# Kernel optimization log

Hardware: AMD Instinct MI355X
Metric: run time of the kernel (lower is better)

## Reference

```python
import jax, jax.numpy as jnp
import numpy as np

EPS = 1e-08
N_NODES = 100000
E_HALF = 3200000  # directed edges before symmetrization


def setup_inputs() -> dict:
    key = jax.random.key(0)
    k1, k2, k3 = jax.random.split(key, 3)
    pos = jax.random.normal(k1, (N_NODES, 3), dtype=jnp.float32)
    phi = jax.random.normal(k2, (N_NODES,), dtype=jnp.float32)
    e = jax.random.randint(k3, (2, E_HALF), 0, N_NODES, dtype=jnp.int32)
    # symmetrize (the torch module calls to_undirected); build undirected edge list
    edge_index = jnp.concatenate([e, e[::-1]], axis=1)  # (2, 2*E_HALF)
    return {"pos": pos, "phi": phi, "edge_index": edge_index}


def reference(pos, phi, edge_index):
    # pos: (N, 3), phi: (N,), edge_index: (2, E) already undirected
    n = pos.shape[0]
    row, col = edge_index[0], edge_index[1]
    dx = pos[col] - pos[row]                      # (E, 3)
    dphi = phi[col] - phi[row]                    # (E,)
    w = 1.0 / (jnp.linalg.norm(dx, axis=1) + EPS) ** 2  # (E,)
    outer = dx[:, :, None] * dx[:, None, :]      # (E, 3, 3)
    A = jax.ops.segment_sum(w[:, None, None] * outer, row, num_segments=n)  # (N,3,3)
    b = jax.ops.segment_sum((w * dphi)[:, None] * dx, row, num_segments=n)  # (N,3)
    A_reg = A + EPS * jnp.eye(3, dtype=pos.dtype)[None, :, :]
    grad_phi = jnp.linalg.solve(A_reg, b[..., None])[..., 0]  # (N,3)
    return grad_phi
```

## Files before the change

### kernel.cpp

```cpp
#include <hip/hip_runtime.h>
#include <hip/hip_bf16.h>
#include <math.h>

#define LSQ_EPS 1e-8f
#define BUCKET_BITS 7
#define BUCKET_SIZE 128
#define NB_MAX 800
#define CAP 8960
#define SCAT_BLOCKS 1024
#define STAGE_CAP 6272
#define VEC_ITERS 4
#define KV 5

__device__ __forceinline__ int hget(const unsigned int* hp, int b) {
    return (int)((hp[b >> 1] >> ((b & 1) * 16)) & 0xFFFFu);
}
__device__ __forceinline__ unsigned int hinc_rank(unsigned int* hp, int b) {
    unsigned int o = atomicAdd(&hp[b >> 1], 1u << ((b & 1) * 16));
    return (o >> ((b & 1) * 16)) & 0xFFFFu;
}

__global__ __launch_bounds__(256, 5) void lsq_scatter_sorted(
    const float* __restrict__ pos, const float* __restrict__ phi,
    const int* __restrict__ eidx, int E, int N, int NB,
    float4* __restrict__ pp4,
    unsigned int* __restrict__ region, int* __restrict__ g_cursor)
{
    __shared__ unsigned int staged[STAGE_CAP];
    __shared__ unsigned int histp[NB_MAX / 2];
    __shared__ unsigned short base16[NB_MAX];
    __shared__ unsigned short sstart16[NB_MAX];

    const int tid = threadIdx.x;
    const int E2 = E >> 1;

    for (int i = blockIdx.x * 256 + tid; i < N; i += SCAT_BLOCKS * 256)
        pp4[i] = make_float4(pos[3 * i + 0], pos[3 * i + 1], pos[3 * i + 2], phi[i]);

    int chunk = (E2 + SCAT_BLOCKS - 1) / SCAT_BLOCKS;
    chunk = (chunk + 3) & ~3;
    const int start = blockIdx.x * chunk;
    const int end = min(start + chunk, E2);
    if (start >= E2) return;

    for (int t = tid; t < NB_MAX / 2; t += 256) histp[t] = 0;
    __syncthreads();

    const int nvec = (end - start) & ~3;
    unsigned int rkA[VEC_ITERS][4];
    int4 rA[VEC_ITERS], cA[VEC_ITERS];
#pragma unroll
    for (int k = 0; k < VEC_ITERS; ++k) {
        int e = start + (tid << 2) + (k << 10);
        if (e < start + nvec) {
            int4 r = *(const int4*)(eidx + e);
            int4 c = *(const int4*)(eidx + E + e);
            rA[k] = r;
            cA[k] = c;
            rkA[k][0] = hinc_rank(histp, r.x >> BUCKET_BITS) |
                        (hinc_rank(histp, c.x >> BUCKET_BITS) << 16);
            rkA[k][1] = hinc_rank(histp, r.y >> BUCKET_BITS) |
                        (hinc_rank(histp, c.y >> BUCKET_BITS) << 16);
            rkA[k][2] = hinc_rank(histp, r.z >> BUCKET_BITS) |
                        (hinc_rank(histp, c.z >> BUCKET_BITS) << 16);
            rkA[k][3] = hinc_rank(histp, r.w >> BUCKET_BITS) |
                        (hinc_rank(histp, c.w >> BUCKET_BITS) << 16);
        }
    }
    unsigned int rkT = 0;
    int trow = 0, tcol = 0;
    const int tcnt = (end - start) - nvec;
    if (tid < tcnt) {
        int e = start + nvec + tid;
        trow = eidx[e];
        tcol = eidx[E + e];
        rkT = hinc_rank(histp, trow >> BUCKET_BITS) |
              (hinc_rank(histp, tcol >> BUCKET_BITS) << 16);
    }
    __syncthreads();

    int bs0 = 0, bs1 = 0, bs2 = 0, bs3 = 0;
    {
        int b = tid;
        if (b < NB) { int c = hget(histp, b); if (c > 0) bs0 = atomicAdd(&g_cursor[b], c); }
        b += 256;
        if (b < NB) { int c = hget(histp, b); if (c > 0) bs1 = atomicAdd(&g_cursor[b], c); }
        b += 256;
        if (b < NB) { int c = hget(histp, b); if (c > 0) bs2 = atomicAdd(&g_cursor[b], c); }
        b += 256;
        if (b < NB) { int c = hget(histp, b); if (c > 0) bs3 = atomicAdd(&g_cursor[b], c); }
    }
    if (tid < 64) {
        int carry = 0;
        for (int bi = 0; bi < NB; bi += 64) {
            int b = bi + tid;
            int c = (b < NB) ? hget(histp, b) : 0;
            int x = c;
#pragma unroll
            for (int d = 1; d < 64; d <<= 1) {
                int y = __shfl_up(x, d, 64);
                if (tid >= d) x += y;
            }
            if (b < NB) sstart16[b] = (unsigned short)(carry + x - c);
            carry += __shfl(x, 63, 64);
        }
    }
    asm volatile("s_waitcnt lgkmcnt(0)" ::: "memory");
    __builtin_amdgcn_s_barrier();

#pragma unroll
    for (int k = 0; k < VEC_ITERS; ++k) {
        int e = start + (tid << 2) + (k << 10);
        if (e < start + nvec) {
            int rr[4] = {rA[k].x, rA[k].y, rA[k].z, rA[k].w};
            int cc[4] = {cA[k].x, cA[k].y, cA[k].z, cA[k].w};
#pragma unroll
            for (int q = 0; q < 4; ++q) {
                int b1 = rr[q] >> BUCKET_BITS;
                int s1 = (int)sstart16[b1] + (int)(rkA[k][q] & 0xFFFFu);
                staged[s1] = ((unsigned int)(rr[q] & (BUCKET_SIZE - 1)) << 17) | (unsigned int)cc[q];
                int b2 = cc[q] >> BUCKET_BITS;
                int s2 = (int)sstart16[b2] + (int)(rkA[k][q] >> 16);
                staged[s2] = ((unsigned int)(cc[q] & (BUCKET_SIZE - 1)) << 17) | (unsigned int)rr[q];
            }
        }
    }
    if (tid < tcnt) {
        int b1 = trow >> BUCKET_BITS;
        staged[(int)sstart16[b1] + (int)(rkT & 0xFFFFu)] =
            ((unsigned int)(trow & (BUCKET_SIZE - 1)) << 17) | (unsigned int)tcol;
        int b2 = tcol >> BUCKET_BITS;
        staged[(int)sstart16[b2] + (int)(rkT >> 16)] =
            ((unsigned int)(tcol & (BUCKET_SIZE - 1)) << 17) | (unsigned int)trow;
    }

    if (tid < NB)       base16[tid]       = (unsigned short)min(bs0, 65535);
    if (tid + 256 < NB) base16[tid + 256] = (unsigned short)min(bs1, 65535);
    if (tid + 512 < NB) base16[tid + 512] = (unsigned short)min(bs2, 65535);
    if (tid + 768 < NB) base16[tid + 768] = (unsigned short)min(bs3, 65535);
    __syncthreads();

    {
        const int wv = tid >> 6, ln = tid & 63;
        const int grp = ln >> 3;
        const int sub = ln & 7;
        for (int b = wv * 8 + grp; b < NB; b += 32) {
            int cnt_b = hget(histp, b);
            if (cnt_b == 0) continue;
            int src = (int)sstart16[b];
            int dst = (int)base16[b];
            int kmax = min(cnt_b, CAP - dst);
            if (kmax <= 0) continue;
            unsigned int* dstp = region + (size_t)b * CAP + dst;
            const unsigned int* srcp = staged + src;
            for (int j = sub; j < kmax; j += 8)
                dstp[j] = srcp[j];
        }
    }
}

#define LSQ_ACC(qv)                                                            \
    {                                                                          \
        float dx = (qv).x - me.x;                                              \
        float dy = (qv).y - me.y;                                              \
        float dz = (qv).z - me.z;                                              \
        float dphi = (qv).w - me.w;                                            \
        float nn = sqrtf(dx * dx + dy * dy + dz * dz) + LSQ_EPS;               \
        float w = 1.0f / (nn * nn);                                            \
        float wd = w * dphi;                                                   \
        a00 += w * dx * dx; a01 += w * dx * dy; a02 += w * dx * dz;            \
        a11 += w * dy * dy; a12 += w * dy * dz; a22 += w * dz * dz;            \
        bb0 += wd * dx;     bb1 += wd * dy;     bb2 += wd * dz;                \
    }

__global__ __launch_bounds__(512, 8) void lsq_bucket_reduce(
    const float4* __restrict__ pp4,
    const unsigned int* __restrict__ region, const int* __restrict__ g_cursor,
    float* __restrict__ out, int N)
{
    __shared__ unsigned int sorted32[CAP];
    __shared__ int cnt[BUCKET_SIZE];
    __shared__ int startx[BUCKET_SIZE];

    const int b = blockIdx.x;
    const int tid = threadIdx.x;
    const int node_base = b << BUCKET_BITS;

    if (tid < BUCKET_SIZE) cnt[tid] = 0;
    __syncthreads();

    int count = g_cursor[b];
    if (count > CAP) count = CAP;
    const unsigned int* reg = region + (size_t)b * CAP;

    uint4 pcv[KV];
#pragma unroll
    for (int k = 0; k < KV; ++k) {
        int i = (tid << 2) + (k << 11);
        if (i < count) {
            uint4 p = *(const uint4*)(reg + i);
            unsigned int o0 = (unsigned int)atomicAdd(&cnt[p.x >> 17], 1);
            pcv[k].x = p.x | (o0 << 24);
            if (i + 1 < count) {
                unsigned int o1 = (unsigned int)atomicAdd(&cnt[p.y >> 17], 1);
                pcv[k].y = p.y | (o1 << 24);
            }
            if (i + 2 < count) {
                unsigned int o2 = (unsigned int)atomicAdd(&cnt[p.z >> 17], 1);
                pcv[k].z = p.z | (o2 << 24);
            }
            if (i + 3 < count) {
                unsigned int o3 = (unsigned int)atomicAdd(&cnt[p.w >> 17], 1);
                pcv[k].w = p.w | (o3 << 24);
            }
        }
    }
    __syncthreads();

    if (tid < 64) {
        int c0 = cnt[tid];
        int c1 = cnt[tid + 64];
        int x0 = c0, x1 = c1;
#pragma unroll
        for (int d = 1; d < 64; d <<= 1) {
            int y0 = __shfl_up(x0, d, 64);
            int y1 = __shfl_up(x1, d, 64);
            if (tid >= d) { x0 += y0; x1 += y1; }
        }
        int tot0 = __shfl(x0, 63, 64);
        startx[tid] = x0 - c0;
        startx[tid + 64] = tot0 + x1 - c1;
    }
    __syncthreads();

#pragma unroll
    for (int k = 0; k < KV; ++k) {
        int i = (tid << 2) + (k << 11);
        if (i < count) {
            unsigned int p0 = pcv[k].x;
            sorted32[startx[(p0 >> 17) & 0x7Fu] + (int)(p0 >> 24)] = p0 & 0x1FFFFu;
            if (i + 1 < count) {
                unsigned int p1 = pcv[k].y;
                sorted32[startx[(p1 >> 17) & 0x7Fu] + (int)(p1 >> 24)] = p1 & 0x1FFFFu;
            }
            if (i + 2 < count) {
                unsigned int p2 = pcv[k].z;
                sorted32[startx[(p2 >> 17) & 0x7Fu] + (int)(p2 >> 24)] = p2 & 0x1FFFFu;
            }
            if (i + 3 < count) {
                unsigned int p3 = pcv[k].w;
                sorted32[startx[(p3 >> 17) & 0x7Fu] + (int)(p3 >> 24)] = p3 & 0x1FFFFu;
            }
        }
    }
    __syncthreads();

    const int n = tid >> 2;
    const int qid = tid & 3;
    int node = node_base + n;
    float4 me = pp4[node < N ? node : 0];
    const int s = startx[n];
    const int cN = cnt[n];
    int lo = s + (cN * qid) / 4;
    const int hi = s + (cN * (qid + 1)) / 4;

    float a00 = 0, a01 = 0, a02 = 0, a11 = 0, a12 = 0, a22 = 0;
    float bb0 = 0, bb1 = 0, bb2 = 0;

    int i = lo;
    for (; i + 3 < hi; i += 4) {
        int c0 = (int)sorted32[i];
        int c1 = (int)sorted32[i + 1];
        int c2 = (int)sorted32[i + 2];
        int c3 = (int)sorted32[i + 3];
        float4 q0 = pp4[c0];
        float4 q1 = pp4[c1];
        float4 q2 = pp4[c2];
        float4 q3 = pp4[c3];
        LSQ_ACC(q0); LSQ_ACC(q1); LSQ_ACC(q2); LSQ_ACC(q3);
    }
    for (; i < hi; ++i) {
        int c0 = (int)sorted32[i];
        float4 q0 = pp4[c0];
        LSQ_ACC(q0);
    }

    a00 += __shfl_down(a00, 1); a01 += __shfl_down(a01, 1);
    a02 += __shfl_down(a02, 1); a11 += __shfl_down(a11, 1);
    a12 += __shfl_down(a12, 1); a22 += __shfl_down(a22, 1);
    bb0 += __shfl_down(bb0, 1); bb1 += __shfl_down(bb1, 1);
    bb2 += __shfl_down(bb2, 1);
    a00 += __shfl_down(a00, 2); a01 += __shfl_down(a01, 2);
    a02 += __shfl_down(a02, 2); a11 += __shfl_down(a11, 2);
    a12 += __shfl_down(a12, 2); a22 += __shfl_down(a22, 2);
    bb0 += __shfl_down(bb0, 2); bb1 += __shfl_down(bb1, 2);
    bb2 += __shfl_down(bb2, 2);

    if (qid == 0 && node < N) {
        double a00d = (double)a00 + 1e-8;
        double a01d = (double)a01;
        double a02d = (double)a02;
        double a11d = (double)a11 + 1e-8;
        double a12d = (double)a12;
        double a22d = (double)a22 + 1e-8;
        double b0 = (double)bb0;
        double b1 = (double)bb1;
        double b2 = (double)bb2;

        double c00 = a11d * a22d - a12d * a12d;
        double c01 = a02d * a12d - a01d * a22d;
        double c02 = a01d * a12d - a02d * a11d;
        double c11 = a00d * a22d - a02d * a02d;
        double c12 = a01d * a02d - a00d * a12d;
        double c22 = a00d * a11d - a01d * a01d;

        double det = a00d * c00 + a01d * c01 + a02d * c02;
        double inv = 1.0 / det;

        out[node * 3 + 0] = (float)((c00 * b0 + c01 * b1 + c02 * b2) * inv);
        out[node * 3 + 1] = (float)((c01 * b0 + c11 * b1 + c12 * b2) * inv);
        out[node * 3 + 2] = (float)((c02 * b0 + c12 * b1 + c22 * b2) * inv);
    }
}

__global__ void lsq_edge_scatter(const float* __restrict__ pos,
                                 const float* __restrict__ phi,
                                 const int* __restrict__ eidx,
                                 float* __restrict__ acc,
                                 int E) {
    int e = blockIdx.x * blockDim.x + threadIdx.x;
    if (e >= E) return;
    int r = eidx[e];
    int c = eidx[E + e];
    float dx = pos[3 * c + 0] - pos[3 * r + 0];
    float dy = pos[3 * c + 1] - pos[3 * r + 1];
    float dz = pos[3 * c + 2] - pos[3 * r + 2];
    float dphi = phi[c] - phi[r];
    float n = sqrtf(dx * dx + dy * dy + dz * dz) + LSQ_EPS;
    float w = 1.0f / (n * n);
    float wd = w * dphi;
    float* a = acc + (size_t)r * 9;
    unsafeAtomicAdd(a + 0, w * dx * dx);
    unsafeAtomicAdd(a + 1, w * dx * dy);
    unsafeAtomicAdd(a + 2, w * dx * dz);
    unsafeAtomicAdd(a + 3, w * dy * dy);
    unsafeAtomicAdd(a + 4, w * dy * dz);
    unsafeAtomicAdd(a + 5, w * dz * dz);
    unsafeAtomicAdd(a + 6, wd * dx);
    unsafeAtomicAdd(a + 7, wd * dy);
    unsafeAtomicAdd(a + 8, wd * dz);
}

__global__ void lsq_solve3(const float* __restrict__ acc,
                           float* __restrict__ out,
                           int N) {
    int i = blockIdx.x * blockDim.x + threadIdx.x;
    if (i >= N) return;
    const float* a = acc + (size_t)i * 9;
    double a00 = (double)a[0] + 1e-8;
    double a01 = (double)a[1];
    double a02 = (double)a[2];
    double a11 = (double)a[3] + 1e-8;
    double a12 = (double)a[4];
    double a22 = (double)a[5] + 1e-8;
    double b0 = (double)a[6];
    double b1 = (double)a[7];
    double b2 = (double)a[8];
    double c00 = a11 * a22 - a12 * a12;
    double c01 = a02 * a12 - a01 * a22;
    double c02 = a01 * a12 - a02 * a11;
    double c11 = a00 * a22 - a02 * a02;
    double c12 = a01 * a02 - a00 * a12;
    double c22 = a00 * a11 - a01 * a01;
    double det = a00 * c00 + a01 * c01 + a02 * c02;
    double inv = 1.0 / det;
    out[3 * i + 0] = (float)((c00 * b0 + c01 * b1 + c02 * b2) * inv);
    out[3 * i + 1] = (float)((c01 * b0 + c11 * b1 + c12 * b2) * inv);
    out[3 * i + 2] = (float)((c02 * b0 + c12 * b1 + c22 * b2) * inv);
}

extern "C" void kernel_launch(void* const* d_in, const int* in_sizes, int n_in,
                              void* d_out, int out_size, void* d_ws, size_t ws_size,
                              hipStream_t stream) {
    const float* pos = (const float*)d_in[0];
    const float* phi = (const float*)d_in[1];
    const int* eidx = (const int*)d_in[2];
    float* out = (float*)d_out;

    int N = in_sizes[0] / 3;
    int E = in_sizes[2] / 2;
    int NB = (N + BUCKET_SIZE - 1) >> BUCKET_BITS;

    size_t region_bytes = (size_t)NB * CAP * sizeof(unsigned int);
    size_t pp4_bytes = (size_t)N * sizeof(float4);
    size_t need = region_bytes + pp4_bytes + (size_t)NB * sizeof(int);

    int chunk = ((E / 2) + SCAT_BLOCKS - 1) / SCAT_BLOCKS;
    chunk = (chunk + 3) & ~3;
    bool stage_ok = (2 * chunk) <= STAGE_CAP;

    if (NB <= NB_MAX && ws_size >= need && (E & 3) == 0 && stage_ok) {
        unsigned int* region = (unsigned int*)d_ws;
        float4* pp4 = (float4*)((char*)d_ws + region_bytes);
        int* g_cursor = (int*)((char*)d_ws + region_bytes + pp4_bytes);

        hipMemsetAsync(g_cursor, 0, (size_t)NB * sizeof(int), stream);
        lsq_scatter_sorted<<<SCAT_BLOCKS, 256, 0, stream>>>(
            pos, phi, eidx, E, N, NB, pp4, region, g_cursor);
        lsq_bucket_reduce<<<NB, 512, 0, stream>>>(pp4, region, g_cursor, out, N);
    } else {
        float* acc = (float*)d_ws;
        hipMemsetAsync(acc, 0, (size_t)N * 9 * sizeof(float), stream);
        int threads = 256;
        lsq_edge_scatter<<<(E + threads - 1) / threads, threads, 0, stream>>>(pos, phi, eidx, acc, E);
        lsq_solve3<<<(N + threads - 1) / threads, threads, 0, stream>>>(acc, out, N);
    }
}
```

Measured before the change: 169.6 us.

## Double node bucket size to 256 and use two lanes per node in reduce

Widens each bucket from 128 to 256 nodes, which halves the number of buckets and global cursor atomics in the scatter pass and enlarges each region. The reduce kernel now sorts a larger region per block, uses a looped prefix scan over 256 counters, and assigns two lanes per node instead of four. The aim is fewer blocks and less scatter-side overhead. In exchange the reduce uses more shared memory and registers (KV=9, launch bounds lowered to 4 blocks), which cuts occupancy and gives each lane a longer serial gather loop.

```diff
diff --git a/kernel.cpp b/kernel.cpp
--- a/kernel.cpp
+++ b/kernel.cpp
@@ -3,14 +3,14 @@
 #include <math.h>
 
 #define LSQ_EPS 1e-8f
-#define BUCKET_BITS 7
-#define BUCKET_SIZE 128
-#define NB_MAX 800
-#define CAP 8960
+#define BUCKET_BITS 8
+#define BUCKET_SIZE 256
+#define NB_MAX 400
+#define CAP 17408
 #define SCAT_BLOCKS 1024
 #define STAGE_CAP 6272
 #define VEC_ITERS 4
-#define KV 5
+#define KV 9
 
 __device__ __forceinline__ int hget(const unsigned int* hp, int b) {
     return (int)((hp[b >> 1] >> ((b & 1) * 16)) & 0xFFFFu);
@@ -79,16 +79,12 @@
     }
     __syncthreads();
 
-    int bs0 = 0, bs1 = 0, bs2 = 0, bs3 = 0;
+    int bs0 = 0, bs1 = 0;
     {
         int b = tid;
         if (b < NB) { int c = hget(histp, b); if (c > 0) bs0 = atomicAdd(&g_cursor[b], c); }
         b += 256;
         if (b < NB) { int c = hget(histp, b); if (c > 0) bs1 = atomicAdd(&g_cursor[b], c); }
-        b += 256;
-        if (b < NB) { int c = hget(histp, b); if (c > 0) bs2 = atomicAdd(&g_cursor[b], c); }
-        b += 256;
-        if (b < NB) { int c = hget(histp, b); if (c > 0) bs3 = atomicAdd(&g_cursor[b], c); }
     }
     if (tid < 64) {
         int carry = 0;
@@ -136,15 +132,13 @@
 
     if (tid < NB)       base16[tid]       = (unsigned short)min(bs0, 65535);
     if (tid + 256 < NB) base16[tid + 256] = (unsigned short)min(bs1, 65535);
-    if (tid + 512 < NB) base16[tid + 512] = (unsigned short)min(bs2, 65535);
-    if (tid + 768 < NB) base16[tid + 768] = (unsigned short)min(bs3, 65535);
     __syncthreads();
 
     {
         const int wv = tid >> 6, ln = tid & 63;
-        const int grp = ln >> 3;
-        const int sub = ln & 7;
-        for (int b = wv * 8 + grp; b < NB; b += 32) {
+        const int grp = ln >> 4;
+        const int sub = ln & 15;
+        for (int b = wv * 4 + grp; b < NB; b += 16) {
             int cnt_b = hget(histp, b);
             if (cnt_b == 0) continue;
             int src = (int)sstart16[b];
@@ -153,7 +147,7 @@
             if (kmax <= 0) continue;
             unsigned int* dstp = region + (size_t)b * CAP + dst;
             const unsigned int* srcp = staged + src;
-            for (int j = sub; j < kmax; j += 8)
+            for (int j = sub; j < kmax; j += 16)
                 dstp[j] = srcp[j];
         }
     }
@@ -173,7 +167,7 @@
         bb0 += wd * dx;     bb1 += wd * dy;     bb2 += wd * dz;                \
     }
 
-__global__ __launch_bounds__(512, 8) void lsq_bucket_reduce(
+__global__ __launch_bounds__(512, 4) void lsq_bucket_reduce(
     const float4* __restrict__ pp4,
     const unsigned int* __restrict__ region, const int* __restrict__ g_cursor,
     float* __restrict__ out, int N)
@@ -200,36 +194,36 @@
         if (i < count) {
             uint4 p = *(const uint4*)(reg + i);
             unsigned int o0 = (unsigned int)atomicAdd(&cnt[p.x >> 17], 1);
-            pcv[k].x = p.x | (o0 << 24);
+            pcv[k].x = p.x | (o0 << 25);
             if (i + 1 < count) {
                 unsigned int o1 = (unsigned int)atomicAdd(&cnt[p.y >> 17], 1);
-                pcv[k].y = p.y | (o1 << 24);
+                pcv[k].y = p.y | (o1 << 25);
             }
             if (i + 2 < count) {
                 unsigned int o2 = (unsigned int)atomicAdd(&cnt[p.z >> 17], 1);
-                pcv[k].z = p.z | (o2 << 24);
+                pcv[k].z = p.z | (o2 << 25);
             }
             if (i + 3 < count) {
                 unsigned int o3 = (unsigned int)atomicAdd(&cnt[p.w >> 17], 1);
-                pcv[k].w = p.w | (o3 << 24);
+                pcv[k].w = p.w | (o3 << 25);
             }
         }
     }
     __syncthreads();
 
     if (tid < 64) {
-        int c0 = cnt[tid];
-        int c1 = cnt[tid + 64];
-        int x0 = c0, x1 = c1;
-#pragma unroll
-        for (int d = 1; d < 64; d <<= 1) {
-            int y0 = __shfl_up(x0, d, 64);
-            int y1 = __shfl_up(x1, d, 64);
-            if (tid >= d) { x0 += y0; x1 += y1; }
-        }
-        int tot0 = __shfl(x0, 63, 64);
-        startx[tid] = x0 - c0;
-        startx[tid + 64] = tot0 + x1 - c1;
+        int carry = 0;
+        for (int base = 0; base < BUCKET_SIZE; base += 64) {
+            int c = cnt[base + tid];
+            int x = c;
+#pragma unroll
+            for (int d = 1; d < 64; d <<= 1) {
+                int y = __shfl_up(x, d, 64);
+                if (tid >= d) x += y;
+            }
+            startx[base + tid] = carry + x - c;
+            carry += __shfl(x, 63, 64);
+        }
     }
     __syncthreads();
 
@@ -238,31 +232,31 @@
         int i = (tid << 2) + (k << 11);
         if (i < count) {
             unsigned int p0 = pcv[k].x;
-            sorted32[startx[(p0 >> 17) & 0x7Fu] + (int)(p0 >> 24)] = p0 & 0x1FFFFu;
+            sorted32[startx[(p0 >> 17) & 0xFFu] + (int)(p0 >> 25)] = p0 & 0x1FFFFu;
             if (i + 1 < count) {
                 unsigned int p1 = pcv[k].y;
-                sorted32[startx[(p1 >> 17) & 0x7Fu] + (int)(p1 >> 24)] = p1 & 0x1FFFFu;
+                sorted32[startx[(p1 >> 17) & 0xFFu] + (int)(p1 >> 25)] = p1 & 0x1FFFFu;
             }
             if (i + 2 < count) {
                 unsigned int p2 = pcv[k].z;
-                sorted32[startx[(p2 >> 17) & 0x7Fu] + (int)(p2 >> 24)] = p2 & 0x1FFFFu;
+                sorted32[startx[(p2 >> 17) & 0xFFu] + (int)(p2 >> 25)] = p2 & 0x1FFFFu;
             }
             if (i + 3 < count) {
                 unsigned int p3 = pcv[k].w;
-                sorted32[startx[(p3 >> 17) & 0x7Fu] + (int)(p3 >> 24)] = p3 & 0x1FFFFu;
-            }
-        }
-    }
-    __syncthreads();
-
-    const int n = tid >> 2;
-    const int qid = tid & 3;
+                sorted32[startx[(p3 >> 17) & 0xFFu] + (int)(p3 >> 25)] = p3 & 0x1FFFFu;
+            }
+        }
+    }
+    __syncthreads();
+
+    const int n = tid >> 1;
+    const int qid = tid & 1;
     int node = node_base + n;
     float4 me = pp4[node < N ? node : 0];
     const int s = startx[n];
     const int cN = cnt[n];
-    int lo = s + (cN * qid) / 4;
-    const int hi = s + (cN * (qid + 1)) / 4;
+    int lo = s + (cN * qid) / 2;
+    const int hi = s + (cN * (qid + 1)) / 2;
 
     float a00 = 0, a01 = 0, a02 = 0, a11 = 0, a12 = 0, a22 = 0;
     float bb0 = 0, bb1 = 0, bb2 = 0;
@@ -290,11 +284,6 @@
     a12 += __shfl_down(a12, 1); a22 += __shfl_down(a22, 1);
     bb0 += __shfl_down(bb0, 1); bb1 += __shfl_down(bb1, 1);
     bb2 += __shfl_down(bb2, 1);
-    a00 += __shfl_down(a00, 2); a01 += __shfl_down(a01, 2);
-    a02 += __shfl_down(a02, 2); a11 += __shfl_down(a11, 2);
-    a12 += __shfl_down(a12, 2); a22 += __shfl_down(a22, 2);
-    bb0 += __shfl_down(bb0, 2); bb1 += __shfl_down(bb1, 2);
-    bb2 += __shfl_down(bb2, 2);
 
     if (qid == 0 && node < N) {
         double a00d = (double)a00 + 1e-8;
```

Result: faster. 163.8 us (-3.4%).
